# Kernel optimization log

Hardware: AMD Instinct MI355X
Metric: run time of the kernel (lower is better)

Reference implementation:

```python
import jax, jax.numpy as jnp
import numpy as np

MIN_LEN = 4      # g.min_word_length
MAX_LEN = 10     # g.max_word_length
THRESH = 0.05    # g.init_threshold
NEG = -1e9


def setup_inputs() -> dict:
    key = jax.random.key(0)
    ks = jax.random.split(key, 6)
    B, L, F, D, U, V = 16, 64, 60, 256, 600, 10000
    x = jax.random.normal(ks[0], (B, L, F), jnp.float32)            # batch dense feat matrix
    unit_feats = jax.random.normal(ks[1], (U, F), jnp.float32)      # per-unit features
    W = jax.random.normal(ks[2], (F, D), jnp.float32) * 0.1         # FeatEmbedding weight
    lengths = jax.random.randint(ks[3], (B,), MIN_LEN, L + 1)       # sentence lengths
    indexed_segments = jax.random.randint(ks[4], (V, MAX_LEN), 0, U)  # vocab -> unit ids
    vocab_length = jax.random.randint(ks[5], (V,), MIN_LEN, MAX_LEN + 1)
    return dict(x=x, unit_feats=unit_feats, W=W, lengths=lengths,
                indexed_segments=indexed_segments, vocab_length=vocab_length)


def reference(x, unit_feats, W, lengths, indexed_segments, vocab_length):
    B, L, _ = x.shape
    V, J = indexed_segments.shape
    # embedding: features -> char_emb space
    word_repr = x @ W                 # [B, L, D]
    unit_repr = unit_feats @ W        # [U, D]
    # cosine similarity between every segment position and every unit
    wn = word_repr / (jnp.linalg.norm(word_repr, axis=-1, keepdims=True) + 1e-8)
    un = unit_repr / (jnp.linalg.norm(unit_repr, axis=-1, keepdims=True) + 1e-8)
    sim = jnp.einsum('bld,ud->blu', wn, un)  # [B, L, U]
    # pad so span gathers past the end read zeros (masked later by `viable`)
    sim_pad = jnp.pad(sim, ((0, 0), (0, J), (0, 0)))
    # accumulate per-position unit scores along each vocab word's unit sequence
    acc = jnp.zeros((B, L, V), sim.dtype)
    per_len = []
    for j in range(J):  # fixed small loop over word-length positions
        # sim at start+j for unit indexed_segments[v, j] -> [B, L, V]
        s_j = sim_pad[:, j:j + L, :][:, :, indexed_segments[:, j]]
        acc = acc + s_j
        if j + 1 >= MIN_LEN:
            per_len.append(acc / (j + 1))  # length-normalized match score
    scores = jnp.stack(per_len, axis=2)  # [B, len_s=L, len_e=E, V]
    E = scores.shape[2]
    k = jnp.arange(E) + MIN_LEN                          # candidate word lengths
    ends = jnp.arange(L)[:, None] + k[None, :] - 1        # [L, E]
    viable = ends[None] < lengths[:, None, None]          # [B, L, E]
    len_match = vocab_length[None, None, None, :] == k[None, None, :, None]
    mask = viable[..., None] & len_match                  # [B, L, E, V]
    masked = jnp.where(mask, scores, NEG)
    # best vocab word per span candidate
    value = masked.max(axis=-1)                           # [B, L, E]
    matched_vocab = masked.argmax(axis=-1)                # [B, L, E]
    matched = value > THRESH
    # best span candidate per batch element (eval path: hard max)
    flat = value.reshape(B, -1)                           # [B, L*E]
    best_inds = flat.argmax(axis=-1)
    best_scores = flat.max(axis=-1)
    best_starts = best_inds // E
    best_ends = best_inds % E + best_starts + MIN_LEN - 1
    any_matched = matched.reshape(B, -1).any(axis=-1)
    best_vocab = jnp.take_along_axis(matched_vocab.reshape(B, -1), best_inds[:, None], axis=1)[:, 0]
    return best_scores, best_starts, best_ends, any_matched, best_vocab
```

## Files before the change

kernel.cpp:

```cpp
#include <hip/hip_runtime.h>
#include <math.h>

#define BB 16
#define LL 64
#define FF 60
#define DD 256
#define UU 600
#define VV 10000
#define JMAX 10
#define MINL 4
#define EE 7
#define NEG (-1e9f)
#define TH 0.05f
#define BCAP 10240

#define UNT_OFF   0
#define WNT_OFF   163840
#define SIM_OFF   425984
#define CNT_OFF   1040384
#define SRT_OFF   1040392
#define VAL_OFF   1613832
#define VOC_OFF   1628168

__global__ __launch_bounds__(256) void k_prep(const int* __restrict__ seg,
                                              const int* __restrict__ vlen,
                                              const float* __restrict__ x,
                                              const float* __restrict__ uf,
                                              const float* __restrict__ W,
                                              unsigned int* __restrict__ cnt,
                                              unsigned int* __restrict__ srt,
                                              float* __restrict__ unT,
                                              float* __restrict__ wnT) {
    __shared__ unsigned long long sP[4][2];
    __shared__ int wTab[4][8];
    __shared__ int sBase[8];
    int blk = blockIdx.x;
    if (blk < 40) {
        int tid  = threadIdx.x;
        int lane = tid & 63;
        int w    = tid >> 6;
        int v    = blk * 256 + tid;

        unsigned long long p0 = 0, p1 = 0;
        int lim = blk * 256;
        for (int i = tid; i < lim; i += 256) {
            int e2 = vlen[i] - MINL;
            if (e2 < 4) p0 += 1ull << (e2 * 16);
            else        p1 += 1ull << ((e2 - 4) * 16);
        }
#pragma unroll
        for (int m = 32; m > 0; m >>= 1) {
            p0 += __shfl_xor(p0, m, 64);
            p1 += __shfl_xor(p1, m, 64);
        }
        if (lane == 0) { sP[w][0] = p0; sP[w][1] = p1; }

        int e = (v < VV) ? (vlen[v] - MINL) : -1;
        unsigned long long below = (lane == 0) ? 0ull : (~0ull >> (64 - lane));
        unsigned long long mym = 0;
#pragma unroll
        for (int b2 = 0; b2 < EE; ++b2) {
            unsigned long long m = __ballot(e == b2);
            if (lane == 0) wTab[w][b2] = (int)__popcll(m);
            if (e == b2) mym = m;
        }
        __syncthreads();
        if (tid < EE) {
            unsigned long long q0 = sP[0][0] + sP[1][0] + sP[2][0] + sP[3][0];
            unsigned long long q1 = sP[0][1] + sP[1][1] + sP[2][1] + sP[3][1];
            int base = (tid < 4) ? (int)((q0 >> (tid * 16)) & 0xffffull)
                                 : (int)((q1 >> ((tid - 4) * 16)) & 0xffffull);
            sBase[tid] = base;
            if (blk == 39)
                cnt[tid] = (unsigned)(base + wTab[0][tid] + wTab[1][tid]
                                           + wTab[2][tid] + wTab[3][tid]);
        }
        __syncthreads();

        if (v < VV) {
            int prior = sBase[e];
#pragma unroll
            for (int w2 = 0; w2 < 4; ++w2) if (w2 < w) prior += wTab[w2][e];
            unsigned pos = (unsigned)(prior + (int)__popcll(mym & below));

            const int* s = seg + v * JMAX;
            unsigned int t[10];
#pragma unroll
            for (int j = 0; j < JMAX; ++j) t[j] = (unsigned int)(s[j] * 13 + j);
            unsigned int* dst = srt + ((size_t)e * BCAP + pos) * 8;
            uint4 qa, qb;
            qa.x = t[0] | (t[1] << 16);
            qa.y = t[2] | (t[3] << 16);
            qa.z = t[4] | (t[5] << 16);
            qa.w = t[6] | (t[7] << 16);
            qb.x = t[8] | (t[9] << 16);
            qb.y = (unsigned int)v;
            qb.z = 0; qb.w = 0;
            ((uint4*)dst)[0] = qa;
            ((uint4*)dst)[1] = qb;
        }
    } else {
        int w = threadIdx.x >> 6;
        int lane = threadIdx.x & 63;
        int id = (blk - 40) * 4 + w;
        const float* row;
        float* outB;
        int stride, col;
        if (id < UU) { row = uf + id * FF; outB = unT; stride = 640;  col = id; }
        else { int bl = id - UU; row = x + bl * FF; outB = wnT; stride = 1024; col = bl; }

        float r0 = 0.f, r1 = 0.f, r2 = 0.f, r3 = 0.f;
#pragma unroll 4
        for (int f = 0; f < FF; ++f) {
            float xv = row[f];
            r0 += xv * W[f * DD + lane];
            r1 += xv * W[f * DD + lane + 64];
            r2 += xv * W[f * DD + lane + 128];
            r3 += xv * W[f * DD + lane + 192];
        }
        float ss = r0 * r0 + r1 * r1 + r2 * r2 + r3 * r3;
#pragma unroll
        for (int m = 32; m > 0; m >>= 1) ss += __shfl_xor(ss, m, 64);
        float inv = 1.0f / (sqrtf(ss) + 1e-8f);
        outB[(lane      ) * stride + col] = r0 * inv;
        outB[(lane +  64) * stride + col] = r1 * inv;
        outB[(lane + 128) * stride + col] = r2 * inv;
        outB[(lane + 192) * stride + col] = r3 * inv;
    }
}

__global__ __launch_bounds__(320) void k_sim(const float* __restrict__ unT,
                                             const float* __restrict__ wnT,
                                             const int* __restrict__ lengths,
                                             float* __restrict__ sim) {
    int blk = blockIdx.x;
    int b  = blk >> 5;
    int r  = blk & 31;
    int l0 = (r >> 1) * 4;
    if (l0 >= lengths[b]) return;
    int uh = r & 1;
    int bl0 = b * 64 + l0;
    int u = uh * 320 + threadIdx.x;

    float a0 = 0.f, a1 = 0.f, a2 = 0.f, a3 = 0.f;
#pragma unroll 8
    for (int d = 0; d < DD; ++d) {
        float4 wv = *(const float4*)(wnT + d * 1024 + bl0);
        float v  = unT[d * 640 + u];
        a0 += wv.x * v;
        a1 += wv.y * v;
        a2 += wv.z * v;
        a3 += wv.w * v;
    }
    if (u < UU) {
        sim[(bl0 + 0) * UU + u] = a0;
        sim[(bl0 + 1) * UU + u] = a1;
        sim[(bl0 + 2) * UU + u] = a2;
        sim[(bl0 + 3) * UU + u] = a3;
    }
}

template<int K>
__device__ __forceinline__ void seg_pass4(const unsigned int* __restrict__ srt,
                                          const float* __restrict__ lds,
                                          int e, int r0, int r1, int lane, int wave,
                                          float (*redS)[8], int (*redV)[8]) {
    float s0 = -1e30f, s1 = -1e30f, s2 = -1e30f, s3 = -1e30f;
    int w0 = VV, w1 = VV, w2 = VV, w3 = VV;
    for (int p = r0 + lane; p < r1; p += 64) {
        const uint4* pp = (const uint4*)(srt + ((size_t)e * BCAP + p) * 8);
        uint4 qa = pp[0];
        uint4 qb = pp[1];
        unsigned int tw[5] = {qa.x, qa.y, qa.z, qa.w, qb.x};
        int v = (int)qb.y;
        float a0 = 0.f, a1 = 0.f, a2 = 0.f, a3 = 0.f;
#pragma unroll
        for (int j = 0; j < K; ++j) {
            int idx = (int)((tw[j >> 1] >> ((j & 1) * 16)) & 0xffffu);
            a0 += lds[idx];
            a1 += lds[idx + 1];
            a2 += lds[idx + 2];
            a3 += lds[idx + 3];
        }
        bool p0 = (a0 > s0) || (a0 == s0 && v < w0);
        bool p1 = (a1 > s1) || (a1 == s1 && v < w1);
        bool p2 = (a2 > s2) || (a2 == s2 && v < w2);
        bool p3 = (a3 > s3) || (a3 == s3 && v < w3);
        s0 = p0 ? a0 : s0;  w0 = p0 ? v : w0;
        s1 = p1 ? a1 : s1;  w1 = p1 ? v : w1;
        s2 = p2 ? a2 : s2;  w2 = p2 ? v : w2;
        s3 = p3 ? a3 : s3;  w3 = p3 ? v : w3;
    }
#pragma unroll
    for (int off = 32; off > 0; off >>= 1) {
        float os; int ov;
        os = __shfl_down(s0, off, 64); ov = __shfl_down(w0, off, 64);
        if (os > s0 || (os == s0 && ov < w0)) { s0 = os; w0 = ov; }
        os = __shfl_down(s1, off, 64); ov = __shfl_down(w1, off, 64);
        if (os > s1 || (os == s1 && ov < w1)) { s1 = os; w1 = ov; }
        os = __shfl_down(s2, off, 64); ov = __shfl_down(w2, off, 64);
        if (os > s2 || (os == s2 && ov < w2)) { s2 = os; w2 = ov; }
        os = __shfl_down(s3, off, 64); ov = __shfl_down(w3, off, 64);
        if (os > s3 || (os == s3 && ov < w3)) { s3 = os; w3 = ov; }
    }
    if (lane == 0) {
        redS[e * 4 + 0][wave] = s0; redV[e * 4 + 0][wave] = w0;
        redS[e * 4 + 1][wave] = s1; redV[e * 4 + 1][wave] = w1;
        redS[e * 4 + 2][wave] = s2; redV[e * 4 + 2][wave] = w2;
        redS[e * 4 + 3][wave] = s3; redV[e * 4 + 3][wave] = w3;
    }
}

__global__ __launch_bounds__(512, 2) void k_score(const float* __restrict__ sim,
                                                  const unsigned int* __restrict__ srt,
                                                  const unsigned int* __restrict__ cnt,
                                                  const int* __restrict__ lengths,
                                                  float* __restrict__ val,
                                                  int* __restrict__ voc) {
    __shared__ float lds[UU * 13];
    __shared__ float redS[28][8];
    __shared__ int   redV[28][8];

    int blk = blockIdx.x;
    int half = blk >> 8;
    int rest = blk & 255;
    int b  = rest >> 4;
    int l0 = (rest & 15) * 4;
    int tid = threadIdx.x;
    int len = lengths[b];

    if (l0 + MINL - 1 >= len) {
        if (tid < 28) {
            int e  = tid >> 2;
            int dl = tid & 3;
            int o = (half * BB * LL + b * 64 + l0 + dl) * EE + e;
            val[o] = NEG;
            voc[o] = 0;
        }
        return;
    }

    if (tid < 224) {
        redS[tid >> 3][tid & 7] = -1e30f;
        redV[tid >> 3][tid & 7] = VV;
    }
    for (int i = tid; i < 13 * 150; i += 512) {
        int r = i / 150;
        int c = i - r * 150;
        int m = l0 + r;
        float4 v4;
        if (m < LL) v4 = *(const float4*)(sim + (size_t)(b * 64 + m) * UU + 4 * c);
        else        v4 = make_float4(0.f, 0.f, 0.f, 0.f);
        int u0 = 4 * c;
        lds[(u0 + 0) * 13 + r] = v4.x;
        lds[(u0 + 1) * 13 + r] = v4.y;
        lds[(u0 + 2) * 13 + r] = v4.z;
        lds[(u0 + 3) * 13 + r] = v4.w;
    }
    __syncthreads();

    int wave = tid >> 6, lane = tid & 63;

    unsigned nlo[EE], nhi[EE], Bw[EE];
    unsigned Wtot = 0;
#pragma unroll
    for (int e = 0; e < EE; ++e) {
        unsigned n = cnt[e];
        unsigned lo = half ? (n >> 1) : 0;
        unsigned hi = half ? n : (n >> 1);
        if (l0 + e + MINL - 1 >= len) { lo = 0; hi = 0; }
        nlo[e] = lo; nhi[e] = hi;
        Bw[e] = Wtot;
        Wtot += (hi - lo) * (unsigned)(e + MINL);
    }
    unsigned qlo = (unsigned)(((unsigned long long)Wtot * (unsigned)wave) >> 3);
    unsigned qhi = (unsigned)(((unsigned long long)Wtot * (unsigned)(wave + 1)) >> 3);

#pragma unroll
    for (int e = 0; e < EE; ++e) {
        unsigned K = (unsigned)(e + MINL);
        unsigned segw = (nhi[e] - nlo[e]) * K;
        unsigned Be = Bw[e];
        if (qhi <= Be || qlo >= Be + segw || segw == 0) continue;
        unsigned a = (qlo > Be) ? (qlo - Be) : 0;
        unsigned bb = qhi - Be; if (bb > segw) bb = segw;
        int r0 = (int)(nlo[e] + (a + K - 1) / K);
        int r1 = (int)(nlo[e] + (bb + K - 1) / K);
        if (r1 <= r0) continue;
        switch (e) {
            case 0: seg_pass4<4> (srt, lds, 0, r0, r1, lane, wave, redS, redV); break;
            case 1: seg_pass4<5> (srt, lds, 1, r0, r1, lane, wave, redS, redV); break;
            case 2: seg_pass4<6> (srt, lds, 2, r0, r1, lane, wave, redS, redV); break;
            case 3: seg_pass4<7> (srt, lds, 3, r0, r1, lane, wave, redS, redV); break;
            case 4: seg_pass4<8> (srt, lds, 4, r0, r1, lane, wave, redS, redV); break;
            case 5: seg_pass4<9> (srt, lds, 5, r0, r1, lane, wave, redS, redV); break;
            case 6: seg_pass4<10>(srt, lds, 6, r0, r1, lane, wave, redS, redV); break;
        }
    }
    __syncthreads();

    if (tid < 28) {
        int e  = tid >> 2;
        int dl = tid & 3;
        float s = redS[tid][0];
        int  vv = redV[tid][0];
#pragma unroll
        for (int w2 = 1; w2 < 8; ++w2) {
            float os = redS[tid][w2];
            int   ov = redV[tid][w2];
            if (os > s || (os == s && ov < vv)) { s = os; vv = ov; }
        }
        int lg = l0 + dl;
        int k = e + MINL;
        bool viable = (lg + k - 1) < len;
        float sn = s / (float)k;
        int o = (half * BB * LL + b * 64 + lg) * EE + e;
        val[o] = viable ? sn : NEG;
        voc[o] = viable ? vv : 0;
    }
}

__global__ __launch_bounds__(512) void k_final(const float* __restrict__ val,
                                               const int* __restrict__ voc,
                                               float* __restrict__ out) {
    __shared__ float sS[8];
    __shared__ int   sI[8];
    __shared__ int   sV[8];
    __shared__ int   sA[8];
    int b = blockIdx.x;
    int t = threadIdx.x;
    float s = -3e38f;
    int idx = 1 << 30;
    int vc = 0;
    int any = 0;
    if (t < LL * EE) {
        int o0 = b * LL * EE + t;
        int o1 = BB * LL * EE + o0;
        float s0 = val[o0], s1 = val[o1];
        int   v0 = voc[o0], v1 = voc[o1];
        bool sel = (s1 > s0) || (s1 == s0 && v1 < v0);
        s  = sel ? s1 : s0;
        vc = sel ? v1 : v0;
        idx = t;
        any = (s > TH) ? 1 : 0;
    }
#pragma unroll
    for (int off = 32; off > 0; off >>= 1) {
        float os = __shfl_down(s, off, 64);
        int   oi = __shfl_down(idx, off, 64);
        int   ov = __shfl_down(vc, off, 64);
        int   oa = __shfl_down(any, off, 64);
        if (os > s || (os == s && oi < idx)) { s = os; idx = oi; vc = ov; }
        any |= oa;
    }
    int w = t >> 6, lane = t & 63;
    if (lane == 0) { sS[w] = s; sI[w] = idx; sV[w] = vc; sA[w] = any; }
    __syncthreads();
    if (t == 0) {
        for (int w2 = 1; w2 < 8; ++w2) {
            float os = sS[w2];
            int   oi = sI[w2];
            if (os > s || (os == s && oi < idx)) { s = os; idx = oi; vc = sV[w2]; }
            any |= sA[w2];
        }
        int start = idx / EE;
        int e = idx - start * EE;
        int end = e + start + MINL - 1;
        out[b]      = s;
        out[16 + b] = (float)start;
        out[32 + b] = (float)end;
        out[48 + b] = any ? 1.0f : 0.0f;
        out[64 + b] = (float)vc;
    }
}

extern "C" void kernel_launch(void* const* d_in, const int* in_sizes, int n_in,
                              void* d_out, int out_size, void* d_ws, size_t ws_size,
                              hipStream_t stream) {
    const float* x       = (const float*)d_in[0];
    const float* uf      = (const float*)d_in[1];
    const float* W       = (const float*)d_in[2];
    const int*   lengths = (const int*)d_in[3];
    const int*   seg     = (const int*)d_in[4];
    const int*   vlen    = (const int*)d_in[5];
    float* out = (float*)d_out;
    float* ws  = (float*)d_ws;

    float*        unT = ws + UNT_OFF;
    float*        wnT = ws + WNT_OFF;
    float*        sim = ws + SIM_OFF;
    unsigned int* cnt = (unsigned int*)(ws + CNT_OFF);
    unsigned int* srt = (unsigned int*)(ws + SRT_OFF);
    float*        val = ws + VAL_OFF;
    int*          voc = (int*)(ws + VOC_OFF);

    k_prep<<<446, 256, 0, stream>>>(seg, vlen, x, uf, W, cnt, srt, unT, wnT);
    k_sim<<<512, 320, 0, stream>>>(unT, wnT, lengths, sim);
    k_score<<<512, 512, 0, stream>>>(sim, srt, cnt, lengths, val, voc);
    k_final<<<BB, 512, 0, stream>>>(val, voc, out);
}
```

Baseline: 125.8 us.

## Fuse final reduction into score kernel via packed-key atomicMax and last-block epilogue

Removes the separate k_final launch and the val/voc intermediate buffers. Each score block packs its best (score, span index, vocab) into a monotonic 64-bit key and does an atomicMax per batch element. The last block to finish, found with an atomic done counter, decodes the keys and writes the outputs. This saves one kernel launch and a global round trip. In exchange it adds global atomics and a threadfence, and the any_matched flag is now taken from the best score instead of an explicit OR.

Result: slower. 129.3 us (+2.8%).

```diff
diff --git a/kernel.cpp b/kernel.cpp
--- a/kernel.cpp
+++ b/kernel.cpp
@@ -19,8 +19,8 @@
 #define SIM_OFF   425984
 #define CNT_OFF   1040384
 #define SRT_OFF   1040392
-#define VAL_OFF   1613832
-#define VOC_OFF   1628168
+#define BEST_OFF  1613832
+#define DONE_OFF  1613864
 
 __global__ __launch_bounds__(256) void k_prep(const int* __restrict__ seg,
                                               const int* __restrict__ vlen,
@@ -30,7 +30,9 @@
                                               unsigned int* __restrict__ cnt,
                                               unsigned int* __restrict__ srt,
                                               float* __restrict__ unT,
-                                              float* __restrict__ wnT) {
+                                              float* __restrict__ wnT,
+                                              unsigned long long* __restrict__ best,
+                                              unsigned int* __restrict__ done) {
     __shared__ unsigned long long sP[4][2];
     __shared__ int wTab[4][8];
     __shared__ int sBase[8];
@@ -74,6 +76,10 @@
             if (blk == 39)
                 cnt[tid] = (unsigned)(base + wTab[0][tid] + wTab[1][tid]
                                            + wTab[2][tid] + wTab[3][tid]);
+        }
+        if (blk == 39) {
+            if (tid >= 128 && tid < 144) best[tid - 128] = 0ull;
+            if (tid == 144) *done = 0u;
         }
         __syncthreads();
 
@@ -215,11 +221,13 @@
                                                   const unsigned int* __restrict__ srt,
                                                   const unsigned int* __restrict__ cnt,
                                                   const int* __restrict__ lengths,
-                                                  float* __restrict__ val,
-                                                  int* __restrict__ voc) {
+                                                  unsigned long long* __restrict__ best,
+                                                  unsigned int* __restrict__ done,
+                                                  float* __restrict__ out) {
     __shared__ float lds[UU * 13];
     __shared__ float redS[28][8];
     __shared__ int   redV[28][8];
+    __shared__ int   isLast;
 
     int blk = blockIdx.x;
     int half = blk >> 8;
@@ -228,149 +236,125 @@
     int l0 = (rest & 15) * 4;
     int tid = threadIdx.x;
     int len = lengths[b];
-
-    if (l0 + MINL - 1 >= len) {
+    bool alive = (l0 + MINL - 1 < len);
+
+    if (alive) {
+        if (tid < 224) {
+            redS[tid >> 3][tid & 7] = -1e30f;
+            redV[tid >> 3][tid & 7] = VV;
+        }
+        for (int i = tid; i < 13 * 150; i += 512) {
+            int r = i / 150;
+            int c = i - r * 150;
+            int m = l0 + r;
+            float4 v4;
+            if (m < LL) v4 = *(const float4*)(sim + (size_t)(b * 64 + m) * UU + 4 * c);
+            else        v4 = make_float4(0.f, 0.f, 0.f, 0.f);
+            int u0 = 4 * c;
+            lds[(u0 + 0) * 13 + r] = v4.x;
+            lds[(u0 + 1) * 13 + r] = v4.y;
+            lds[(u0 + 2) * 13 + r] = v4.z;
+            lds[(u0 + 3) * 13 + r] = v4.w;
+        }
+        __syncthreads();
+
+        int wave = tid >> 6, lane = tid & 63;
+
+        unsigned nlo[EE], nhi[EE], Bw[EE];
+        unsigned Wtot = 0;
+#pragma unroll
+        for (int e = 0; e < EE; ++e) {
+            unsigned n = cnt[e];
+            unsigned lo = half ? (n >> 1) : 0;
+            unsigned hi = half ? n : (n >> 1);
+            if (l0 + e + MINL - 1 >= len) { lo = 0; hi = 0; }
+            nlo[e] = lo; nhi[e] = hi;
+            Bw[e] = Wtot;
+            Wtot += (hi - lo) * (unsigned)(e + MINL);
+        }
+        unsigned qlo = (unsigned)(((unsigned long long)Wtot * (unsigned)wave) >> 3);
+        unsigned qhi = (unsigned)(((unsigned long long)Wtot * (unsigned)(wave + 1)) >> 3);
+
+#pragma unroll
+        for (int e = 0; e < EE; ++e) {
+            unsigned K = (unsigned)(e + MINL);
+            unsigned segw = (nhi[e] - nlo[e]) * K;
+            unsigned Be = Bw[e];
+            if (qhi <= Be || qlo >= Be + segw || segw == 0) continue;
+            unsigned a = (qlo > Be) ? (qlo - Be) : 0;
+            unsigned bb = qhi - Be; if (bb > segw) bb = segw;
+            int r0 = (int)(nlo[e] + (a + K - 1) / K);
+            int r1 = (int)(nlo[e] + (bb + K - 1) / K);
+            if (r1 <= r0) continue;
+            switch (e) {
+                case 0: seg_pass4<4> (srt, lds, 0, r0, r1, lane, wave, redS, redV); break;
+                case 1: seg_pass4<5> (srt, lds, 1, r0, r1, lane, wave, redS, redV); break;
+                case 2: seg_pass4<6> (srt, lds, 2, r0, r1, lane, wave, redS, redV); break;
+                case 3: seg_pass4<7> (srt, lds, 3, r0, r1, lane, wave, redS, redV); break;
+                case 4: seg_pass4<8> (srt, lds, 4, r0, r1, lane, wave, redS, redV); break;
+                case 5: seg_pass4<9> (srt, lds, 5, r0, r1, lane, wave, redS, redV); break;
+                case 6: seg_pass4<10>(srt, lds, 6, r0, r1, lane, wave, redS, redV); break;
+            }
+        }
+        __syncthreads();
+
+        unsigned long long key = 0ull;
         if (tid < 28) {
             int e  = tid >> 2;
             int dl = tid & 3;
-            int o = (half * BB * LL + b * 64 + l0 + dl) * EE + e;
-            val[o] = NEG;
-            voc[o] = 0;
-        }
-        return;
-    }
-
-    if (tid < 224) {
-        redS[tid >> 3][tid & 7] = -1e30f;
-        redV[tid >> 3][tid & 7] = VV;
-    }
-    for (int i = tid; i < 13 * 150; i += 512) {
-        int r = i / 150;
-        int c = i - r * 150;
-        int m = l0 + r;
-        float4 v4;
-        if (m < LL) v4 = *(const float4*)(sim + (size_t)(b * 64 + m) * UU + 4 * c);
-        else        v4 = make_float4(0.f, 0.f, 0.f, 0.f);
-        int u0 = 4 * c;
-        lds[(u0 + 0) * 13 + r] = v4.x;
-        lds[(u0 + 1) * 13 + r] = v4.y;
-        lds[(u0 + 2) * 13 + r] = v4.z;
-        lds[(u0 + 3) * 13 + r] = v4.w;
+            float s = redS[tid][0];
+            int  vv = redV[tid][0];
+#pragma unroll
+            for (int w2 = 1; w2 < 8; ++w2) {
+                float os = redS[tid][w2];
+                int   ov = redV[tid][w2];
+                if (os > s || (os == s && ov < vv)) { s = os; vv = ov; }
+            }
+            int lg = l0 + dl;
+            int k = e + MINL;
+            if (lg + k - 1 < len) {
+                float sn = s / (float)k;
+                sn += 0.0f;
+                unsigned int ub  = __float_as_uint(sn);
+                unsigned int enc = (ub & 0x80000000u) ? ~ub : (ub | 0x80000000u);
+                int idx = lg * EE + e;
+                key = ((unsigned long long)enc << 32)
+                    | ((unsigned long long)(unsigned)(511 - idx) << 14)
+                    | (unsigned long long)(unsigned)(16383 - vv);
+            }
+        }
+        if (tid < 64) {
+#pragma unroll
+            for (int off = 32; off > 0; off >>= 1) {
+                unsigned long long ok = __shfl_down(key, off, 64);
+                if (ok > key) key = ok;
+            }
+            if (tid == 0 && key != 0ull) atomicMax(&best[b], key);
+        }
+    }
+
+    if (tid == 0) {
+        __threadfence();
+        unsigned int old = atomicAdd(done, 1u);
+        isLast = (old == 511u) ? 1 : 0;
     }
     __syncthreads();
-
-    int wave = tid >> 6, lane = tid & 63;
-
-    unsigned nlo[EE], nhi[EE], Bw[EE];
-    unsigned Wtot = 0;
-#pragma unroll
-    for (int e = 0; e < EE; ++e) {
-        unsigned n = cnt[e];
-        unsigned lo = half ? (n >> 1) : 0;
-        unsigned hi = half ? n : (n >> 1);
-        if (l0 + e + MINL - 1 >= len) { lo = 0; hi = 0; }
-        nlo[e] = lo; nhi[e] = hi;
-        Bw[e] = Wtot;
-        Wtot += (hi - lo) * (unsigned)(e + MINL);
-    }
-    unsigned qlo = (unsigned)(((unsigned long long)Wtot * (unsigned)wave) >> 3);
-    unsigned qhi = (unsigned)(((unsigned long long)Wtot * (unsigned)(wave + 1)) >> 3);
-
-#pragma unroll
-    for (int e = 0; e < EE; ++e) {
-        unsigned K = (unsigned)(e + MINL);
-        unsigned segw = (nhi[e] - nlo[e]) * K;
-        unsigned Be = Bw[e];
-        if (qhi <= Be || qlo >= Be + segw || segw == 0) continue;
-        unsigned a = (qlo > Be) ? (qlo - Be) : 0;
-        unsigned bb = qhi - Be; if (bb > segw) bb = segw;
-        int r0 = (int)(nlo[e] + (a + K - 1) / K);
-        int r1 = (int)(nlo[e] + (bb + K - 1) / K);
-        if (r1 <= r0) continue;
-        switch (e) {
-            case 0: seg_pass4<4> (srt, lds, 0, r0, r1, lane, wave, redS, redV); break;
-            case 1: seg_pass4<5> (srt, lds, 1, r0, r1, lane, wave, redS, redV); break;
-            case 2: seg_pass4<6> (srt, lds, 2, r0, r1, lane, wave, redS, redV); break;
-            case 3: seg_pass4<7> (srt, lds, 3, r0, r1, lane, wave, redS, redV); break;
-            case 4: seg_pass4<8> (srt, lds, 4, r0, r1, lane, wave, redS, redV); break;
-            case 5: seg_pass4<9> (srt, lds, 5, r0, r1, lane, wave, redS, redV); break;
-            case 6: seg_pass4<10>(srt, lds, 6, r0, r1, lane, wave, redS, redV); break;
-        }
-    }
-    __syncthreads();
-
-    if (tid < 28) {
-        int e  = tid >> 2;
-        int dl = tid & 3;
-        float s = redS[tid][0];
-        int  vv = redV[tid][0];
-#pragma unroll
-        for (int w2 = 1; w2 < 8; ++w2) {
-            float os = redS[tid][w2];
-            int   ov = redV[tid][w2];
-            if (os > s || (os == s && ov < vv)) { s = os; vv = ov; }
-        }
-        int lg = l0 + dl;
-        int k = e + MINL;
-        bool viable = (lg + k - 1) < len;
-        float sn = s / (float)k;
-        int o = (half * BB * LL + b * 64 + lg) * EE + e;
-        val[o] = viable ? sn : NEG;
-        voc[o] = viable ? vv : 0;
-    }
-}
-
-__global__ __launch_bounds__(512) void k_final(const float* __restrict__ val,
-                                               const int* __restrict__ voc,
-                                               float* __restrict__ out) {
-    __shared__ float sS[8];
-    __shared__ int   sI[8];
-    __shared__ int   sV[8];
-    __shared__ int   sA[8];
-    int b = blockIdx.x;
-    int t = threadIdx.x;
-    float s = -3e38f;
-    int idx = 1 << 30;
-    int vc = 0;
-    int any = 0;
-    if (t < LL * EE) {
-        int o0 = b * LL * EE + t;
-        int o1 = BB * LL * EE + o0;
-        float s0 = val[o0], s1 = val[o1];
-        int   v0 = voc[o0], v1 = voc[o1];
-        bool sel = (s1 > s0) || (s1 == s0 && v1 < v0);
-        s  = sel ? s1 : s0;
-        vc = sel ? v1 : v0;
-        idx = t;
-        any = (s > TH) ? 1 : 0;
-    }
-#pragma unroll
-    for (int off = 32; off > 0; off >>= 1) {
-        float os = __shfl_down(s, off, 64);
-        int   oi = __shfl_down(idx, off, 64);
-        int   ov = __shfl_down(vc, off, 64);
-        int   oa = __shfl_down(any, off, 64);
-        if (os > s || (os == s && oi < idx)) { s = os; idx = oi; vc = ov; }
-        any |= oa;
-    }
-    int w = t >> 6, lane = t & 63;
-    if (lane == 0) { sS[w] = s; sI[w] = idx; sV[w] = vc; sA[w] = any; }
-    __syncthreads();
-    if (t == 0) {
-        for (int w2 = 1; w2 < 8; ++w2) {
-            float os = sS[w2];
-            int   oi = sI[w2];
-            if (os > s || (os == s && oi < idx)) { s = os; idx = oi; vc = sV[w2]; }
-            any |= sA[w2];
-        }
+    if (isLast && tid < BB) {
+        __threadfence();
+        unsigned long long kb = atomicAdd(&best[tid], 0ull);
+        unsigned int enc = (unsigned int)(kb >> 32);
+        unsigned int ub  = (enc & 0x80000000u) ? (enc & 0x7fffffffu) : ~enc;
+        float s  = __uint_as_float(ub);
+        int idx  = 511 - (int)((kb >> 14) & 0x1FFu);
+        int vv   = 16383 - (int)(kb & 0x3FFFu);
         int start = idx / EE;
-        int e = idx - start * EE;
-        int end = e + start + MINL - 1;
-        out[b]      = s;
-        out[16 + b] = (float)start;
-        out[32 + b] = (float)end;
-        out[48 + b] = any ? 1.0f : 0.0f;
-        out[64 + b] = (float)vc;
+        int e     = idx - start * EE;
+        int end   = e + start + MINL - 1;
+        out[tid]      = s;
+        out[16 + tid] = (float)start;
+        out[32 + tid] = (float)end;
+        out[48 + tid] = (s > TH) ? 1.0f : 0.0f;
+        out[64 + tid] = (float)vv;
     }
 }
 
@@ -386,16 +370,16 @@
     float* out = (float*)d_out;
     float* ws  = (float*)d_ws;
 
-    float*        unT = ws + UNT_OFF;
-    float*        wnT = ws + WNT_OFF;
-    float*        sim = ws + SIM_OFF;
-    unsigned int* cnt = (unsigned int*)(ws + CNT_OFF);
-    unsigned int* srt = (unsigned int*)(ws + SRT_OFF);
-    float*        val = ws + VAL_OFF;
-    int*          voc = (int*)(ws + VOC_OFF);
-
-    k_prep<<<446, 256, 0, stream>>>(seg, vlen, x, uf, W, cnt, srt, unT, wnT);
+    float*              unT  = ws + UNT_OFF;
+    float*              wnT  = ws + WNT_OFF;
+    float*              sim  = ws + SIM_OFF;
+    unsigned int*       cnt  = (unsigned int*)(ws + CNT_OFF);
+    unsigned int*       srt  = (unsigned int*)(ws + SRT_OFF);
+    unsigned long long* best = (unsigned long long*)(ws + BEST_OFF);
+    unsigned int*       done = (unsigned int*)(ws + DONE_OFF);
+
+    k_prep<<<446, 256, 0, stream>>>(seg, vlen, x, uf, W, cnt, srt, unT, wnT,
+                                    best, done);
     k_sim<<<512, 320, 0, stream>>>(unT, wnT, lengths, sim);
-    k_score<<<512, 512, 0, stream>>>(sim, srt, cnt, lengths, val, voc);
-    k_final<<<BB, 512, 0, stream>>>(val, voc, out);
-}
+    k_score<<<512, 512, 0, stream>>>(sim, srt, cnt, lengths, best, done, out);
+}
```
